# Performance work log

Measured on AMD Instinct MI355X. Metric: run time of the kernel, lower is better.

## Reference

```python
import jax, jax.numpy as jnp
import numpy as np

NC = 80          # num classes
REG_MAX = 16     # DFL bins
STRIDES = (8, 16, 32)
FEAT_HW = ((80, 80), (40, 40), (20, 20))
MAX_DET = 100
CONF_THRES = 0.25
IOU_THRES = 0.45
PRE_TOPK = 1000  # pre-NMS candidate count (EfficientNMS-style preselection)


def setup_inputs() -> dict:
    key = jax.random.key(0)
    k1, k2, k3 = jax.random.split(key, 3)
    B = 32
    no = 4 * REG_MAX + NC  # 144
    return {
        "p3": jax.random.normal(k1, (B, no, 80, 80), dtype=jnp.float32),
        "p4": jax.random.normal(k2, (B, no, 40, 40), dtype=jnp.float32),
        "p5": jax.random.normal(k3, (B, no, 20, 20), dtype=jnp.float32),
    }


def _make_anchors():
    # grid_cell_offset = 0.5, matching ultralytics make_anchors
    pts, strs = [], []
    for (h, w), s in zip(FEAT_HW, STRIDES):
        sx = jnp.arange(w, dtype=jnp.float32) + 0.5
        sy = jnp.arange(h, dtype=jnp.float32) + 0.5
        yy, xx = jnp.meshgrid(sy, sx, indexing="ij")
        pts.append(jnp.stack([xx.ravel(), yy.ravel()], axis=-1))  # [h*w, 2]
        strs.append(jnp.full((h * w, 1), float(s), dtype=jnp.float32))
    return jnp.concatenate(pts, 0), jnp.concatenate(strs, 0)  # [A,2], [A,1]


def _pairwise_iou(b):
    # b: [K, 4] xyxy
    area = (b[:, 2] - b[:, 0]) * (b[:, 3] - b[:, 1])
    lt = jnp.maximum(b[:, None, :2], b[None, :, :2])
    rb = jnp.minimum(b[:, None, 2:], b[None, :, 2:])
    wh = jnp.clip(rb - lt, 0.0)
    inter = wh[..., 0] * wh[..., 1]
    return inter / (area[:, None] + area[None, :] - inter + 1e-7)


def _nms_single(bxyxy, conf):
    # Greedy class-agnostic NMS over PRE_TOPK score-sorted boxes.
    K = bxyxy.shape[0]
    iou = _pairwise_iou(bxyxy)  # [K, K]
    idx = jnp.arange(K)

    def step(suppressed, xs):
        i, row = xs
        keep = jnp.logical_and(jnp.logical_not(suppressed[i]), conf[i] > 0.0)
        suppressed = jnp.logical_or(suppressed, keep & (row > IOU_THRES) & (idx > i))
        return suppressed, keep

    _, keeps = jax.lax.scan(step, jnp.zeros(K, dtype=bool), (idx, iou))
    return keeps  # [K] bool


def reference(p3, p4, p5):
    feats = [p3, p4, p5]
    B = p3.shape[0]
    no = 4 * REG_MAX + NC
    # concat across scales: [B, no, A]
    x_cat = jnp.concatenate([f.reshape(B, no, -1) for f in feats], axis=2)
    box, cls = x_cat[:, : 4 * REG_MAX], x_cat[:, 4 * REG_MAX:]

    anchors, strd = _make_anchors()  # [A,2], [A,1]
    A = box.shape[-1]

    # DFL: softmax over reg_max bins, expectation with arange weights
    prob = jax.nn.softmax(box.reshape(B, 4, REG_MAX, A), axis=2)
    dist = jnp.einsum("bkra,r->bka", prob, jnp.arange(REG_MAX, dtype=jnp.float32))

    # dist2bbox (xywh) then scale by stride
    anc = anchors.T  # [2, A]
    lt, rb = dist[:, :2], dist[:, 2:]
    x1y1 = anc - lt
    x2y2 = anc + rb
    dbox = jnp.concatenate([(x1y1 + x2y2) * 0.5, x2y2 - x1y1], axis=1) * strd.T  # [B,4,A]

    boxes = dbox.transpose(0, 2, 1)                       # [B, A, 4] xywh
    scores = jax.nn.sigmoid(cls).transpose(0, 2, 1)       # [B, A, NC] (score_activation=1)

    # class-agnostic: best class per box
    conf = scores.max(-1)                                 # [B, A]
    cls_id = jnp.argmax(scores, -1)                       # [B, A]
    conf_m = jnp.where(conf > CONF_THRES, conf, -1.0)

    topv, topi = jax.lax.top_k(conf_m, PRE_TOPK)          # [B, K]
    bsel = jnp.take_along_axis(boxes, topi[..., None], axis=1)  # [B, K, 4]
    cx, cy, w, h = bsel[..., 0], bsel[..., 1], bsel[..., 2], bsel[..., 3]
    bxyxy = jnp.stack([cx - w * 0.5, cy - h * 0.5, cx + w * 0.5, cy + h * 0.5], -1)

    keeps = jax.vmap(_nms_single)(bxyxy, topv)            # [B, K]
    kept_scores = jnp.where(keeps, topv, -1.0)
    dv, di = jax.lax.top_k(kept_scores, MAX_DET)          # [B, MAX_DET]
    valid = dv > 0.0

    det_scores = jnp.where(valid, dv, 0.0)
    det_boxes = jnp.take_along_axis(bxyxy, di[..., None], axis=1) * valid[..., None]
    sel_cls = jnp.take_along_axis(jnp.take_along_axis(cls_id, topi, 1), di, 1)
    det_classes = jnp.where(valid, sel_cls, 0).astype(jnp.int32)
    num_dets = valid.sum(-1, keepdims=True).astype(jnp.int32)
    return num_dets, det_boxes, det_scores, det_classes
```

## Files before the change

### kernel.cpp

```cpp
#include <hip/hip_runtime.h>
#include <math.h>

#define NCLS 80
#define NA 8400
#define NB 32
#define NO 144
#define PRE_TOPK 1000
#define MAX_DET 100

typedef const __attribute__((address_space(1))) void g_void;
typedef __attribute__((address_space(3))) void l_void;

template<int HW, int WDIM, int S>
__device__ __forceinline__ void decode_blk(
    const float* __restrict__ src, int b, int a0, int aoff,
    float* __restrict__ conf, int* __restrict__ clsid, float* __restrict__ box,
    float* s_tile)
{
    int t = threadIdx.x;

    {
        int wv   = t >> 6;
        int lane = t & 63;
        int chl  = wv * 2 + (lane >> 5);
        int aq   = (lane & 31) * 4;
        int aqc  = a0 + aq; if (aqc > HW - 4) aqc = HW - 4;
        const float* gsrc = src + ((size_t)b * NO) * HW + aqc;
        #pragma unroll
        for (int i = 0; i < 9; ++i) {
            const float* gp = gsrc + (size_t)(chl + 16 * i) * HW;
            float* lp = &s_tile[(wv * 2 + 16 * i) * 128];
            __builtin_amdgcn_global_load_lds((g_void*)gp, (l_void*)lp, 16, 0, 0);
        }
    }
    __syncthreads();

    int p = t >> 7;
    int a = t & 127;

    float v[16];
    #pragma unroll
    for (int r = 0; r < 16; ++r) v[r] = s_tile[(p * 16 + r) * 128 + a];
    float mm = v[0];
    #pragma unroll
    for (int r = 1; r < 16; ++r) mm = fmaxf(mm, v[r]);
    float sum = 0.f, d = 0.f;
    #pragma unroll
    for (int r = 0; r < 16; ++r) {
        float e = __expf(v[r] - mm);
        sum += e;
        d += e * (float)r;
    }
    d *= 1.0f / sum;

    float c[20];
    #pragma unroll
    for (int cc = 0; cc < 20; ++cc) c[cc] = s_tile[(64 + p * 20 + cc) * 128 + a];
    float m = c[0]; int ii = 0;
    #pragma unroll
    for (int cc = 1; cc < 20; ++cc) if (c[cc] > m) { m = c[cc]; ii = cc; }

    __syncthreads();

    float* s_dfl = s_tile;
    float* s_mx  = s_tile + 640;
    int*   s_id  = (int*)(s_tile + 1280);
    s_dfl[a * 5 + p] = d;
    s_mx[a * 5 + p]  = m;
    s_id[a * 5 + p]  = p * 20 + ii;
    __syncthreads();

    if (t < 128 && a0 + t < HW) {
        int pos2 = a0 + t;
        float d0 = s_dfl[t * 5 + 0], d1 = s_dfl[t * 5 + 1];
        float d2 = s_dfl[t * 5 + 2], d3 = s_dfl[t * 5 + 3];
        float bm = s_mx[t * 5 + 0]; int bid = s_id[t * 5 + 0];
        float m1 = s_mx[t * 5 + 1]; if (m1 > bm) { bm = m1; bid = s_id[t * 5 + 1]; }
        float m2 = s_mx[t * 5 + 2]; if (m2 > bm) { bm = m2; bid = s_id[t * 5 + 2]; }
        float m3 = s_mx[t * 5 + 3]; if (m3 > bm) { bm = m3; bid = s_id[t * 5 + 3]; }
        float conf_v = 1.0f / (1.0f + __expf(-bm));

        float ax = (float)(pos2 % WDIM) + 0.5f;
        float ay = (float)(pos2 / WDIM) + 0.5f;
        float x1 = ax - d0, y1 = ay - d1;
        float x2 = ax + d2, y2 = ay + d3;
        float cx = ((x1 + x2) * 0.5f) * (float)S;
        float cy = ((y1 + y2) * 0.5f) * (float)S;
        float ww = (x2 - x1) * (float)S;
        float hh = (y2 - y1) * (float)S;

        size_t gid = (size_t)b * NA + aoff + pos2;
        conf[gid]  = conf_v;
        clsid[gid] = bid;
        *(float4*)(box + gid * 4) = make_float4(cx, cy, ww, hh);
    }
}

__global__ __launch_bounds__(512) void k_decode(
    const float* __restrict__ p3, const float* __restrict__ p4, const float* __restrict__ p5,
    float* __restrict__ conf, int* __restrict__ clsid, float* __restrict__ box)
{
    __shared__ float s_tile[NO * 128];
    int blk = blockIdx.x;
    int b = blk / 67;
    int r = blk - b * 67;
    if (r < 50)       decode_blk<6400, 80, 8>(p3, b, r * 128, 0, conf, clsid, box, s_tile);
    else if (r < 63)  decode_blk<1600, 40, 16>(p4, b, (r - 50) * 128, 6400, conf, clsid, box, s_tile);
    else              decode_blk<400, 20, 32>(p5, b, (r - 63) * 128, 8000, conf, clsid, box, s_tile);
}

__device__ __forceinline__ uint32_t ord_bits(float f) {
    uint32_t u = __float_as_uint(f);
    return (u & 0x80000000u) ? ~u : (u | 0x80000000u);
}

__global__ __launch_bounds__(1024) void k_select(
    const float* __restrict__ conf, const float* __restrict__ box, const int* __restrict__ clsid,
    float* __restrict__ topv, float* __restrict__ bxyxy, int* __restrict__ topcls)
{
    int b = blockIdx.x;
    int t = threadIdx.x;
    int lane = t & 63;

    __shared__ uint32_t hist[256];
    __shared__ uint64_t sbuf[1024];
    __shared__ uint32_t s_prefix;
    __shared__ int s_k;
    __shared__ int s_cnt;

    const float* cf = conf + (size_t)b * NA;
    uint32_t kr[9];
    #pragma unroll
    for (int p = 0; p < 9; ++p) {
        int i = t + p * 1024;
        uint32_t k = 0;
        if (i < NA) {
            float c = cf[i];
            float cm = (c > 0.25f) ? c : -1.0f;
            k = ord_bits(cm);
        }
        kr[p] = k;
    }
    if (t == 0) { s_prefix = 0; s_k = PRE_TOPK; s_cnt = 0; }
    sbuf[t] = 0;
    __syncthreads();

    for (int pass = 0; pass < 4; ++pass) {
        int shift = 24 - 8 * pass;
        if (t < 256) hist[t] = 0;
        __syncthreads();
        uint32_t prefix = s_prefix;
        int k = s_k;
        #pragma unroll
        for (int p = 0; p < 9; ++p) {
            int i = t + p * 1024;
            uint32_t key = kr[p];
            bool match = (i < NA) &&
                         ((pass == 0) || (((key ^ prefix) >> (32 - 8 * pass)) == 0));
            uint32_t d = (key >> shift) & 255u;
            if (match) {
                uint64_t m = __ballot(1);
                #pragma unroll
                for (int bb = 0; bb < 8; ++bb) {
                    uint64_t bal = __ballot((d >> bb) & 1u);
                    m &= ((d >> bb) & 1u) ? bal : ~bal;
                }
                if ((m & ((1ull << lane) - 1ull)) == 0ull)
                    atomicAdd(&hist[d], (uint32_t)__popcll(m));
            }
        }
        __syncthreads();
        if (t < 64) {
            uint32_t h0 = hist[4 * t + 0], h1 = hist[4 * t + 1];
            uint32_t h2 = hist[4 * t + 2], h3 = hist[4 * t + 3];
            uint32_t part = h0 + h1 + h2 + h3;
            uint32_t s = part;
            #pragma unroll
            for (int off = 1; off < 64; off <<= 1) {
                uint32_t v = __shfl_down(s, off);
                if (t + off < 64) s += v;
            }
            uint32_t cb3 = s - part;
            uint32_t cb2 = cb3 + h3;
            uint32_t cb1 = cb2 + h2;
            uint32_t cb0 = cb1 + h1;
            uint32_t ku = (uint32_t)k;
            if (cb3 < ku && ku <= cb3 + h3) { s_k = k - (int)cb3; s_prefix = prefix | ((uint32_t)(4 * t + 3) << shift); }
            if (cb2 < ku && ku <= cb2 + h2) { s_k = k - (int)cb2; s_prefix = prefix | ((uint32_t)(4 * t + 2) << shift); }
            if (cb1 < ku && ku <= cb1 + h1) { s_k = k - (int)cb1; s_prefix = prefix | ((uint32_t)(4 * t + 1) << shift); }
            if (cb0 < ku && ku <= cb0 + h0) { s_k = k - (int)cb0; s_prefix = prefix | ((uint32_t)(4 * t + 0) << shift); }
        }
        __syncthreads();
    }

    uint32_t kstar = s_prefix;
    #pragma unroll
    for (int p = 0; p < 9; ++p) {
        int i = t + p * 1024;
        uint32_t key = kr[p];
        if (i < NA && key >= kstar) {
            int pos = atomicAdd(&s_cnt, 1);
            if (pos < 1024) sbuf[pos] = ((uint64_t)key << 14) | (uint64_t)(16383 - i);
        }
    }
    __syncthreads();

    uint64_t v = sbuf[t];
    for (int k = 2; k <= 1024; k <<= 1) {
        for (int j = k >> 1; j > 0; j >>= 1) {
            uint64_t o;
            if (j >= 64) {
                sbuf[t] = v;
                __syncthreads();
                o = sbuf[t ^ j];
                __syncthreads();
            } else {
                o = __shfl_xor((unsigned long long)v, j);
            }
            bool desc  = ((t & k) == 0);
            bool lower = ((t & j) == 0);
            v = (desc == lower) ? (v > o ? v : o) : (v < o ? v : o);
        }
    }

    if (t < PRE_TOPK) {
        uint64_t key = v;
        uint32_t u = (uint32_t)(key >> 14);
        uint32_t fb = (u & 0x80000000u) ? (u ^ 0x80000000u) : ~u;
        float val = __uint_as_float(fb);
        int idx = 16383 - (int)(key & 16383u);
        size_t g = (size_t)b * NA + idx;
        float4 bx = *(const float4*)(box + g * 4);
        float cx = bx.x, cy = bx.y, w = bx.z, h = bx.w;
        size_t o = (size_t)b * PRE_TOPK + t;
        topv[o] = val;
        *(float4*)(bxyxy + o * 4) = make_float4(cx - w * 0.5f, cy - h * 0.5f,
                                                cx + w * 0.5f, cy + h * 0.5f);
        topcls[o] = clsid[g];
    }
}

__device__ __forceinline__ int bslot(int j) { return j + (j >> 6); }

__global__ __launch_bounds__(256) void k_iou(
    const float* __restrict__ bxyxy, unsigned long long* __restrict__ mask)
{
    __shared__ float4 boxes[PRE_TOPK + 16];
    int b = blockIdx.y;
    int t = threadIdx.x;
    const float4* bp = (const float4*)(bxyxy + (size_t)b * PRE_TOPK * 4);
    for (int i = t; i < PRE_TOPK; i += 256) boxes[bslot(i)] = bp[i];
    __syncthreads();

    int r_local = t >> 4, w = t & 15;
    int row = blockIdx.x * 16 + r_local;
    if (row >= PRE_TOPK) return;

    float4 bi = boxes[bslot(row)];
    float area_i = (bi.z - bi.x) * (bi.w - bi.y);
    unsigned long long bits = 0;
    int j0 = w * 64;
    #pragma unroll 4
    for (int jj = 0; jj < 64; ++jj) {
        int j = j0 + jj;
        if (j >= PRE_TOPK) break;
        if (j <= row) continue;
        float4 bj = boxes[bslot(j)];
        float lx = fmaxf(bi.x, bj.x), ly = fmaxf(bi.y, bj.y);
        float rx = fminf(bi.z, bj.z), ry = fminf(bi.w, bj.w);
        float iw = fmaxf(rx - lx, 0.f), ih = fmaxf(ry - ly, 0.f);
        float inter = iw * ih;
        float area_j = (bj.z - bj.x) * (bj.w - bj.y);
        float iou = inter / (area_i + area_j - inter + 1e-7f);
        if (iou > 0.45f) bits |= (1ull << jj);
    }
    mask[((size_t)b * PRE_TOPK + row) * 16 + w] = bits;
}

__global__ __launch_bounds__(1024) void k_nms(
    const unsigned long long* __restrict__ mask, const float* __restrict__ topv,
    const float* __restrict__ bxyxy, const int* __restrict__ topcls,
    float* __restrict__ out)
{
    int b = blockIdx.x;
    int t = threadIdx.x;

    __shared__ __align__(16) unsigned long long smask[PRE_TOPK * 16];
    __shared__ float sv[PRE_TOPK];
    __shared__ unsigned long long s_valid[16];
    __shared__ int kept[MAX_DET];
    __shared__ int s_cnt;

    for (int i = t; i < PRE_TOPK; i += 1024) sv[i] = topv[(size_t)b * PRE_TOPK + i];
    {
        const ulonglong2* src = (const ulonglong2*)(mask + (size_t)b * PRE_TOPK * 16);
        ulonglong2* dst = (ulonglong2*)smask;
        for (int i = t; i < PRE_TOPK * 8; i += 1024) dst[i] = src[i];
    }
    __syncthreads();

    {
        bool pred = (t < PRE_TOPK) && (sv[t] > 0.0f);
        unsigned long long bal = __ballot(pred);
        if ((t & 63) == 0) s_valid[t >> 6] = bal;
    }
    __syncthreads();

    if (t < 64) {
        int w = t;
        unsigned long long supp = 0;
        unsigned long long valid = (w < 16) ? s_valid[w] : 0ull;
        int base = w * 64;
        int cur = -1;
        int cnt = 0;
        while (cnt < MAX_DET) {
            unsigned long long gt;
            if (cur < base)            gt = ~0ull;
            else if (cur - base >= 63) gt = 0ull;
            else                       gt = (~0ull) << (cur - base + 1);
            unsigned long long cand = valid & ~supp & gt;
            int idx = cand ? (base + __builtin_ctzll(cand)) : 0x7FFFFFFF;
            #pragma unroll
            for (int off = 8; off >= 1; off >>= 1) {
                int o = __shfl_xor(idx, off);
                idx = (o < idx) ? o : idx;
            }
            int nxt = __shfl(idx, 0);
            if (nxt == 0x7FFFFFFF) break;
            if (t == 0) kept[cnt] = nxt;
            ++cnt;
            if (w < 16) supp |= smask[nxt * 16 + w];
            cur = nxt;
        }
        if (t == 0) s_cnt = cnt;
    }
    __syncthreads();

    int cnt = s_cnt; if (cnt > MAX_DET) cnt = MAX_DET;
    if (t == 0) out[b] = (float)cnt;
    if (t < MAX_DET) {
        bool valid = t < cnt;
        float bx0 = 0.f, bx1 = 0.f, bx2 = 0.f, bx3 = 0.f, sc = 0.f, cl = 0.f;
        if (valid) {
            int p = kept[t];
            size_t o = (size_t)b * PRE_TOPK + p;
            float4 bb = *(const float4*)(bxyxy + o * 4);
            bx0 = bb.x; bx1 = bb.y; bx2 = bb.z; bx3 = bb.w;
            sc = sv[p];
            cl = (float)topcls[o];
        }
        size_t db = 32 + ((size_t)b * MAX_DET + t) * 4;
        out[db + 0] = bx0; out[db + 1] = bx1; out[db + 2] = bx2; out[db + 3] = bx3;
        out[32 + 12800 + (size_t)b * MAX_DET + t] = sc;
        out[32 + 16000 + (size_t)b * MAX_DET + t] = cl;
    }
}

extern "C" void kernel_launch(void* const* d_in, const int* in_sizes, int n_in,
                              void* d_out, int out_size, void* d_ws, size_t ws_size,
                              hipStream_t stream)
{
    const float* p3 = (const float*)d_in[0];
    const float* p4 = (const float*)d_in[1];
    const float* p5 = (const float*)d_in[2];
    float* out = (float*)d_out;

    char* ws = (char*)d_ws;
    size_t off_mask = 0;
    size_t off_conf = off_mask + (size_t)NB * PRE_TOPK * 16 * 8;
    size_t off_cls  = off_conf + (size_t)NB * NA * 4;
    size_t off_box  = off_cls  + (size_t)NB * NA * 4;
    size_t off_topv = off_box  + (size_t)NB * NA * 4 * 4;
    size_t off_topc = off_topv + (size_t)NB * PRE_TOPK * 4;
    size_t off_bx   = off_topc + (size_t)NB * PRE_TOPK * 4;

    unsigned long long* mask = (unsigned long long*)(ws + off_mask);
    float* conf   = (float*)(ws + off_conf);
    int*   clsid  = (int*)(ws + off_cls);
    float* box    = (float*)(ws + off_box);
    float* topv   = (float*)(ws + off_topv);
    int*   topcls = (int*)(ws + off_topc);
    float* bxyxy  = (float*)(ws + off_bx);

    k_decode<<<NB * 67, 512, 0, stream>>>(p3, p4, p5, conf, clsid, box);
    k_select<<<NB, 1024, 0, stream>>>(conf, box, clsid, topv, bxyxy, topcls);
    k_iou<<<dim3((PRE_TOPK + 15) / 16, NB), 256, 0, stream>>>(bxyxy, mask);
    k_nms<<<NB, 1024, 0, stream>>>(mask, topv, bxyxy, topcls, out);
}
```

Before: 131.3 us.

## Split decode into channel-group partial kernel plus combine kernel

```diff
diff --git a/kernel.cpp b/kernel.cpp
--- a/kernel.cpp
+++ b/kernel.cpp
@@ -11,102 +11,115 @@
 typedef const __attribute__((address_space(1))) void g_void;
 typedef __attribute__((address_space(3))) void l_void;
 
-template<int HW, int WDIM, int S>
-__device__ __forceinline__ void decode_blk(
-    const float* __restrict__ src, int b, int a0, int aoff,
-    float* __restrict__ conf, int* __restrict__ clsid, float* __restrict__ box,
-    float* s_tile)
-{
+__global__ __launch_bounds__(512) void k_part(
+    const float* __restrict__ p3, const float* __restrict__ p4, const float* __restrict__ p5,
+    float* __restrict__ distp, float* __restrict__ clsv, int* __restrict__ clsi)
+{
+    __shared__ float s[16 * 1024];
+    int blk = blockIdx.x;
+    int b = blk / 90;
+    int r = blk - b * 90;
+    int g = r / 10;
+    int tile = r - g * 10;
+
+    const float* src; int HW, a0, aoff;
+    if (tile < 7)      { src = p3; HW = 6400; a0 = tile * 1024;       aoff = 0;    }
+    else if (tile < 9) { src = p4; HW = 1600; a0 = (tile - 7) * 1024; aoff = 6400; }
+    else               { src = p5; HW = 400;  a0 = 0;                 aoff = 8000; }
+    int chbase = (g < 4) ? g * 16 : 64 + (g - 4) * 16;
+
     int t = threadIdx.x;
-
-    {
-        int wv   = t >> 6;
-        int lane = t & 63;
-        int chl  = wv * 2 + (lane >> 5);
-        int aq   = (lane & 31) * 4;
-        int aqc  = a0 + aq; if (aqc > HW - 4) aqc = HW - 4;
-        const float* gsrc = src + ((size_t)b * NO) * HW + aqc;
-        #pragma unroll
-        for (int i = 0; i < 9; ++i) {
-            const float* gp = gsrc + (size_t)(chl + 16 * i) * HW;
-            float* lp = &s_tile[(wv * 2 + 16 * i) * 128];
-            __builtin_amdgcn_global_load_lds((g_void*)gp, (l_void*)lp, 16, 0, 0);
-        }
-    }
-    __syncthreads();
-
-    int p = t >> 7;
-    int a = t & 127;
-
-    float v[16];
+    int wv = t >> 6;
     #pragma unroll
-    for (int r = 0; r < 16; ++r) v[r] = s_tile[(p * 16 + r) * 128 + a];
-    float mm = v[0];
+    for (int i = 0; i < 8; ++i) {
+        int flat = i * 512 + t;
+        int ch = flat >> 8;
+        int q  = flat & 255;
+        int aq = a0 + q * 4; if (aq > HW - 4) aq = HW - 4;
+        const float* gp = src + ((size_t)b * NO + chbase + ch) * HW + aq;
+        float* lp = s + ch * 1024 + (wv & 3) * 256;
+        __builtin_amdgcn_global_load_lds((g_void*)gp, (l_void*)lp, 16, 0, 0);
+    }
+    __syncthreads();
+
     #pragma unroll
-    for (int r = 1; r < 16; ++r) mm = fmaxf(mm, v[r]);
-    float sum = 0.f, d = 0.f;
+    for (int h = 0; h < 2; ++h) {
+        int a = t + h * 512;
+        int ga = a0 + a;
+        bool ok = ga < HW;
+        if (g < 4) {
+            float v[16];
+            #pragma unroll
+            for (int rr = 0; rr < 16; ++rr) v[rr] = s[rr * 1024 + a];
+            float mm = v[0];
+            #pragma unroll
+            for (int rr = 1; rr < 16; ++rr) mm = fmaxf(mm, v[rr]);
+            float sum = 0.f, d = 0.f;
+            #pragma unroll
+            for (int rr = 0; rr < 16; ++rr) {
+                float e = __expf(v[rr] - mm);
+                sum += e;
+                d += e * (float)rr;
+            }
+            d *= 1.0f / sum;
+            if (ok) distp[((size_t)g * NB + b) * NA + aoff + ga] = d;
+        } else {
+            float m = s[a]; int ii = 0;
+            #pragma unroll
+            for (int cc = 1; cc < 16; ++cc) {
+                float x = s[cc * 1024 + a];
+                if (x > m) { m = x; ii = cc; }
+            }
+            if (ok) {
+                size_t o = ((size_t)(g - 4) * NB + b) * NA + aoff + ga;
+                clsv[o] = m;
+                clsi[o] = (g - 4) * 16 + ii;
+            }
+        }
+    }
+}
+
+__global__ __launch_bounds__(256) void k_comb(
+    const float* __restrict__ distp, const float* __restrict__ clsv, const int* __restrict__ clsi,
+    float* __restrict__ conf, int* __restrict__ clsid, float* __restrict__ box)
+{
+    int gid = blockIdx.x * 256 + threadIdx.x;
+    if (gid >= NB * NA) return;
+    int b = gid / NA;
+    int ga = gid - b * NA;
+
+    float d0 = distp[((size_t)0 * NB + b) * NA + ga];
+    float d1 = distp[((size_t)1 * NB + b) * NA + ga];
+    float d2 = distp[((size_t)2 * NB + b) * NA + ga];
+    float d3 = distp[((size_t)3 * NB + b) * NA + ga];
+
+    float bm = clsv[((size_t)0 * NB + b) * NA + ga];
+    int bid   = clsi[((size_t)0 * NB + b) * NA + ga];
     #pragma unroll
-    for (int r = 0; r < 16; ++r) {
-        float e = __expf(v[r] - mm);
-        sum += e;
-        d += e * (float)r;
-    }
-    d *= 1.0f / sum;
-
-    float c[20];
-    #pragma unroll
-    for (int cc = 0; cc < 20; ++cc) c[cc] = s_tile[(64 + p * 20 + cc) * 128 + a];
-    float m = c[0]; int ii = 0;
-    #pragma unroll
-    for (int cc = 1; cc < 20; ++cc) if (c[cc] > m) { m = c[cc]; ii = cc; }
-
-    __syncthreads();
-
-    float* s_dfl = s_tile;
-    float* s_mx  = s_tile + 640;
-    int*   s_id  = (int*)(s_tile + 1280);
-    s_dfl[a * 5 + p] = d;
-    s_mx[a * 5 + p]  = m;
-    s_id[a * 5 + p]  = p * 20 + ii;
-    __syncthreads();
-
-    if (t < 128 && a0 + t < HW) {
-        int pos2 = a0 + t;
-        float d0 = s_dfl[t * 5 + 0], d1 = s_dfl[t * 5 + 1];
-        float d2 = s_dfl[t * 5 + 2], d3 = s_dfl[t * 5 + 3];
-        float bm = s_mx[t * 5 + 0]; int bid = s_id[t * 5 + 0];
-        float m1 = s_mx[t * 5 + 1]; if (m1 > bm) { bm = m1; bid = s_id[t * 5 + 1]; }
-        float m2 = s_mx[t * 5 + 2]; if (m2 > bm) { bm = m2; bid = s_id[t * 5 + 2]; }
-        float m3 = s_mx[t * 5 + 3]; if (m3 > bm) { bm = m3; bid = s_id[t * 5 + 3]; }
-        float conf_v = 1.0f / (1.0f + __expf(-bm));
-
-        float ax = (float)(pos2 % WDIM) + 0.5f;
-        float ay = (float)(pos2 / WDIM) + 0.5f;
-        float x1 = ax - d0, y1 = ay - d1;
-        float x2 = ax + d2, y2 = ay + d3;
-        float cx = ((x1 + x2) * 0.5f) * (float)S;
-        float cy = ((y1 + y2) * 0.5f) * (float)S;
-        float ww = (x2 - x1) * (float)S;
-        float hh = (y2 - y1) * (float)S;
-
-        size_t gid = (size_t)b * NA + aoff + pos2;
-        conf[gid]  = conf_v;
-        clsid[gid] = bid;
-        *(float4*)(box + gid * 4) = make_float4(cx, cy, ww, hh);
-    }
-}
-
-__global__ __launch_bounds__(512) void k_decode(
-    const float* __restrict__ p3, const float* __restrict__ p4, const float* __restrict__ p5,
-    float* __restrict__ conf, int* __restrict__ clsid, float* __restrict__ box)
-{
-    __shared__ float s_tile[NO * 128];
-    int blk = blockIdx.x;
-    int b = blk / 67;
-    int r = blk - b * 67;
-    if (r < 50)       decode_blk<6400, 80, 8>(p3, b, r * 128, 0, conf, clsid, box, s_tile);
-    else if (r < 63)  decode_blk<1600, 40, 16>(p4, b, (r - 50) * 128, 6400, conf, clsid, box, s_tile);
-    else              decode_blk<400, 20, 32>(p5, b, (r - 63) * 128, 8000, conf, clsid, box, s_tile);
+    for (int g = 1; g < 5; ++g) {
+        float m = clsv[((size_t)g * NB + b) * NA + ga];
+        int  id = clsi[((size_t)g * NB + b) * NA + ga];
+        if (m > bm) { bm = m; bid = id; }
+    }
+    float conf_v = 1.0f / (1.0f + __expf(-bm));
+
+    int pos, WDIM; float S;
+    if (ga < 6400)      { pos = ga;        WDIM = 80; S = 8.f;  }
+    else if (ga < 8000) { pos = ga - 6400; WDIM = 40; S = 16.f; }
+    else                { pos = ga - 8000; WDIM = 20; S = 32.f; }
+
+    float ax = (float)(pos % WDIM) + 0.5f;
+    float ay = (float)(pos / WDIM) + 0.5f;
+    float x1 = ax - d0, y1 = ay - d1;
+    float x2 = ax + d2, y2 = ay + d3;
+    float cx = ((x1 + x2) * 0.5f) * S;
+    float cy = ((y1 + y2) * 0.5f) * S;
+    float ww = (x2 - x1) * S;
+    float hh = (y2 - y1) * S;
+
+    conf[gid]  = conf_v;
+    clsid[gid] = bid;
+    *(float4*)(box + (size_t)gid * 4) = make_float4(cx, cy, ww, hh);
 }
 
 __device__ __forceinline__ uint32_t ord_bits(float f) {
@@ -373,6 +386,9 @@
     size_t off_topv = off_box  + (size_t)NB * NA * 4 * 4;
     size_t off_topc = off_topv + (size_t)NB * PRE_TOPK * 4;
     size_t off_bx   = off_topc + (size_t)NB * PRE_TOPK * 4;
+    size_t off_dst  = off_bx   + (size_t)NB * PRE_TOPK * 4 * 4;
+    size_t off_clv  = off_dst  + (size_t)4 * NB * NA * 4;
+    size_t off_cli  = off_clv  + (size_t)5 * NB * NA * 4;
 
     unsigned long long* mask = (unsigned long long*)(ws + off_mask);
     float* conf   = (float*)(ws + off_conf);
@@ -381,8 +397,12 @@
     float* topv   = (float*)(ws + off_topv);
     int*   topcls = (int*)(ws + off_topc);
     float* bxyxy  = (float*)(ws + off_bx);
-
-    k_decode<<<NB * 67, 512, 0, stream>>>(p3, p4, p5, conf, clsid, box);
+    float* distp  = (float*)(ws + off_dst);
+    float* clsv   = (float*)(ws + off_clv);
+    int*   clsi   = (int*)(ws + off_cli);
+
+    k_part<<<NB * 90, 512, 0, stream>>>(p3, p4, p5, distp, clsv, clsi);
+    k_comb<<<(NB * NA + 255) / 256, 256, 0, stream>>>(distp, clsv, clsi, conf, clsid, box);
     k_select<<<NB, 1024, 0, stream>>>(conf, box, clsid, topv, bxyxy, topcls);
     k_iou<<<dim3((PRE_TOPK + 15) / 16, NB), 256, 0, stream>>>(bxyxy, mask);
     k_nms<<<NB, 1024, 0, stream>>>(mask, topv, bxyxy, topcls, out);
```

Measured after the change: 136.4 us. 1.04x slower.
